# Kernel tuning notes

Hardware: AMD Instinct MI355X
Metric: run time of the kernel (lower is better)

The kernel has to match this reference:

```python
import jax, jax.numpy as jnp
import numpy as np

B, T, C, H = 128, 256, 1024, 64


def setup_inputs() -> dict:
    key = jax.random.key(0)
    k1, k2, k3, k4 = jax.random.split(key, 4)
    # Glorot-ish scale for weights
    s = 1.0 / np.sqrt(C)
    return {
        "x": jax.random.normal(k1, (B, T, C), dtype=jnp.float32),
        "Wk": jax.random.normal(k2, (C, H), dtype=jnp.float32) * s,
        "Wq": jax.random.normal(k3, (C, H), dtype=jnp.float32) * s,
        "Wv": jax.random.normal(k4, (C, H), dtype=jnp.float32) * s,
    }


def reference(x, Wk, Wq, Wv):
    # Projections (no bias, matching use_bias=False)
    k = jnp.einsum("btc,ch->bth", x, Wk)  # [B,T,H]
    q = jnp.einsum("btc,ch->bth", x, Wq)
    v = jnp.einsum("btc,ch->bth", x, Wv)
    scale = k.shape[-1] ** -0.5
    wei = jnp.einsum("bth,bsh->bts", q, k) * scale  # [B,T,T]
    t = x.shape[1]
    causal = jnp.tril(jnp.ones((t, t), dtype=bool))
    wei = jnp.where(causal, wei, -jnp.inf)
    wei = jax.nn.softmax(wei, axis=-1)
    # dropout is identity at inference
    out = jnp.einsum("bts,bsh->bth", wei, v)  # [B,T,H]
    return out
```

## Files before the change

### kernel.cpp

```cpp
#include <hip/hip_runtime.h>
#include <hip/hip_bf16.h>

typedef __bf16 v8bf __attribute__((ext_vector_type(8)));
typedef float f32x16 __attribute__((ext_vector_type(16)));
typedef unsigned int uint;
typedef unsigned short ushort;

#define GLOAD16(gsrc, ldst)                                                       \
  __builtin_amdgcn_global_load_lds(                                               \
      (const __attribute__((address_space(1))) unsigned int*)(gsrc),              \
      (__attribute__((address_space(3))) unsigned int*)(ldst), 16, 0, 0)

__device__ inline f32x16 zero16() {
  f32x16 z;
#pragma unroll
  for (int i = 0; i < 16; i++) z[i] = 0.f;
  return z;
}

__device__ inline uint pack_bf16(float a, float b) {
  union { __bf16 h[2]; uint u; } c;
  c.h[0] = (__bf16)a;
  c.h[1] = (__bf16)b;
  return c.u;
}

__global__ void prep_wt(const float* __restrict__ Wq, const float* __restrict__ Wk,
                        const float* __restrict__ Wv, char* __restrict__ Wt_s) {
  __shared__ __bf16 tile[64][74];
  const int mat = blockIdx.x >> 4;
  const int c0 = (blockIdx.x & 15) * 64;
  const float* src = (mat == 0) ? Wq : (mat == 1) ? Wk : Wv;
  const int t = threadIdx.x;
  {
    const int r = t >> 2;
    const int ch = (t & 3) * 16;
    const float4* s4 = (const float4*)(src + (size_t)(c0 + r) * 64 + ch);
#pragma unroll
    for (int j = 0; j < 4; j++) {
      float4 f = s4[j];
      tile[r][ch + 4 * j + 0] = (__bf16)f.x;
      tile[r][ch + 4 * j + 1] = (__bf16)f.y;
      tile[r][ch + 4 * j + 2] = (__bf16)f.z;
      tile[r][ch + 4 * j + 3] = (__bf16)f.w;
    }
  }
  __syncthreads();
  const int h = t >> 2;
  const int cc = (t & 3) * 16;
  union { __bf16 o[16]; uint4 u[2]; } pk;
#pragma unroll
  for (int j = 0; j < 16; j++) pk.o[j] = tile[cc + j][h];
  const int n = mat * 64 + h;
  char* base = Wt_s + (size_t)n * 2048 + (c0 >> 6) * 128;
  const int bc = cc * 2;
  *(uint4*)(base + ((bc) ^ ((n & 7) << 4))) = pk.u[0];
  *(uint4*)(base + ((bc + 16) ^ ((n & 7) << 4))) = pk.u[1];
}

__launch_bounds__(256, 2)
__global__ void proj_kernel(const float* __restrict__ x, const char* __restrict__ Wt_s,
                            __bf16* __restrict__ KQV) {
  __shared__ char lds[65536];
  char* A0 = lds;
  char* A1 = lds + 8192;
  char* W0 = lds + 16384;
  char* W1 = lds + 40960;

  const int tid = threadIdx.x;
  const int lane = tid & 63;
  const int wave = tid >> 6;
  const int wm = wave >> 1;
  const int wn = wave & 1;
  const int row0 = blockIdx.x * 64;

  const int sr = tid >> 2;
  const int sc = tid & 3;
  const float4* xp = (const float4*)(x + (size_t)(row0 + sr) * 1024 + sc * 16);

  f32x16 acc[3];
#pragma unroll
  for (int i = 0; i < 3; i++) acc[i] = zero16();

  float4 s0[4], s1[4], s2[4], s3[4];

#define SB __builtin_amdgcn_sched_barrier(0)

#define LOADA(rr, t)                                                              \
  {                                                                               \
    _Pragma("unroll") for (int j = 0; j < 4; j++) rr[j] = xp[(t) * 16 + j];       \
  }

#define GW(t, Wbuf)                                                               \
  {                                                                               \
    _Pragma("unroll") for (int j = 0; j < 6; j++) {                               \
      int idx = wave * 64 + j * 256 + lane;                                       \
      GLOAD16(Wt_s + (size_t)(idx >> 3) * 2048 + (t) * 128 + (idx & 7) * 16,      \
              Wbuf + wave * 1024 + j * 4096);                                     \
    }                                                                             \
  }

#define CVTWRITE(rr, Abuf)                                                        \
  {                                                                               \
    union { __bf16 h[16]; uint4 u[2]; } cv;                                       \
    _Pragma("unroll") for (int j = 0; j < 4; j++) {                               \
      cv.h[4 * j + 0] = (__bf16)rr[j].x;                                          \
      cv.h[4 * j + 1] = (__bf16)rr[j].y;                                          \
      cv.h[4 * j + 2] = (__bf16)rr[j].z;                                          \
      cv.h[4 * j + 3] = (__bf16)rr[j].w;                                          \
    }                                                                             \
    *(uint4*)(Abuf + sr * 128 + ((sc * 32) ^ ((sr & 7) << 4))) = cv.u[0];         \
    *(uint4*)(Abuf + sr * 128 + ((sc * 32 + 16) ^ ((sr & 7) << 4))) = cv.u[1];    \
  }

#define MMA(Abuf, Wbuf)                                                           \
  {                                                                               \
    _Pragma("unroll") for (int ks = 0; ks < 4; ks++) {                            \
      int arow = wm * 32 + (lane & 31);                                           \
      int kb = ks * 32 + ((lane >> 5) << 4);                                      \
      v8bf av = *(const v8bf*)(Abuf + arow * 128 + (kb ^ ((arow & 7) << 4)));     \
      _Pragma("unroll") for (int nf = 0; nf < 3; nf++) {                          \
        int brow = wn * 96 + nf * 32 + (lane & 31);                               \
        v8bf bv = *(const v8bf*)(Wbuf + brow * 128 + (kb ^ ((brow & 7) << 4)));   \
        acc[nf] = __builtin_amdgcn_mfma_f32_32x32x16_bf16(av, bv, acc[nf], 0, 0, 0); \
      }                                                                           \
    }                                                                             \
  }

#define BAR4                                                                      \
  do {                                                                            \
    asm volatile("s_waitcnt vmcnt(4) lgkmcnt(0)" ::: "memory");                   \
    __builtin_amdgcn_s_barrier();                                                 \
    SB;                                                                           \
  } while (0)
#define BAR0                                                                      \
  do {                                                                            \
    asm volatile("s_waitcnt vmcnt(0) lgkmcnt(0)" ::: "memory");                   \
    __builtin_amdgcn_s_barrier();                                                 \
    SB;                                                                           \
  } while (0)

#define STEP(T, SI, SC_, ACUR, WCUR, ANXT, WNXT)                                  \
  GW(T + 1, WNXT);                                                                \
  SB;                                                                             \
  LOADA(SI, T + 2);                                                               \
  SB;                                                                             \
  MMA(ACUR, WCUR);                                                                \
  CVTWRITE(SC_, ANXT);                                                            \
  BAR4;

  GW(0, W0);
  SB;
  LOADA(s0, 0);
  LOADA(s1, 1);
  SB;
  CVTWRITE(s0, A0);
  BAR4;

  STEP(0, s2, s1, A0, W0, A1, W1)
  STEP(1, s3, s2, A1, W1, A0, W0)
  STEP(2, s0, s3, A0, W0, A1, W1)
  STEP(3, s1, s0, A1, W1, A0, W0)
  STEP(4, s2, s1, A0, W0, A1, W1)
  STEP(5, s3, s2, A1, W1, A0, W0)
  STEP(6, s0, s3, A0, W0, A1, W1)
  STEP(7, s1, s0, A1, W1, A0, W0)
  STEP(8, s2, s1, A0, W0, A1, W1)
  STEP(9, s3, s2, A1, W1, A0, W0)
  STEP(10, s0, s3, A0, W0, A1, W1)
  STEP(11, s1, s0, A1, W1, A0, W0)
  STEP(12, s2, s1, A0, W0, A1, W1)
  STEP(13, s3, s2, A1, W1, A0, W0)
  GW(15, W1);
  SB;
  MMA(A0, W0);
  CVTWRITE(s3, A1);
  BAR0;
  MMA(A1, W1);

#pragma unroll
  for (int nf = 0; nf < 3; nf++) {
#pragma unroll
    for (int r = 0; r < 16; r++) {
      int row = row0 + wm * 32 + (r & 3) + ((r >> 2) << 3) + ((lane >> 5) << 2);
      int col = wn * 96 + nf * 32 + (lane & 31);
      KQV[(size_t)row * 192 + col] = (__bf16)acc[nf][r];
    }
  }
#undef STEP
#undef BAR4
#undef BAR0
#undef LOADA
#undef GW
#undef CVTWRITE
#undef MMA
#undef SB
}

__launch_bounds__(256, 1)
__global__ void attn_kernel(const __bf16* __restrict__ KQV, float* __restrict__ out) {
  __shared__ uint4 lds4[81920 / 16];
  char* Klds = (char*)lds4;
  char* Vlds = (char*)lds4 + 32768;
  char* Qlds = (char*)lds4 + 65536;

  const int tid = threadIdx.x;
  const int lane = tid & 63;
  const int wave = tid >> 6;
  const int b = blockIdx.x >> 1;
  const int half = blockIdx.x & 1;
  const int bt0 = half * 128;
  const size_t base = (size_t)b * 256 * 192;

  {
    int s = tid;
    const uint4* src = (const uint4*)(KQV + base + (size_t)s * 192 + 64);
#pragma unroll
    for (int i = 0; i < 8; i++) {
      uint4 v = src[i];
      int byte = s * 128 + ((i * 16) ^ ((s & 7) << 4));
      *(uint4*)(Klds + byte) = v;
    }
  }
  {
    int s = tid;
    const uint4* src = (const uint4*)(KQV + base + (size_t)s * 192 + 128);
#pragma unroll
    for (int i = 0; i < 8; i++) {
      uint4 v = src[i];
      const ushort* e = (const ushort*)&v;
#pragma unroll
      for (int j = 0; j < 8; j++) {
        int h = i * 8 + j;
        int byte = h * 512 + ((s * 2) ^ ((h & 7) << 4));
        *(ushort*)(Vlds + byte) = e[j];
      }
    }
  }
#pragma unroll
  for (int i = 0; i < 4; i++) {
    int c = tid + i * 256;
    int r = c >> 3, cc = c & 7;
    uint4 v = *(const uint4*)(KQV + base + (size_t)(bt0 + r) * 192 + cc * 8);
    int byte = r * 128 + ((cc * 16) ^ ((r & 7) << 4));
    *(uint4*)(Qlds + byte) = v;
  }
  __syncthreads();

  const int t0 = bt0 + wave * 32;
  const int tg = t0 + (lane & 31);
  const int nf = (t0 >> 5) + 1;

  f32x16 sacc[8];
#pragma unroll
  for (int sf = 0; sf < 8; sf++) {
    f32x16 sv = zero16();
    if (sf < nf) {
#pragma unroll
      for (int ks = 0; ks < 4; ks++) {
        int kbyte = ks * 32 + ((lane >> 5) << 4);
        int krow = sf * 32 + (lane & 31);
        v8bf a = *(const v8bf*)(Klds + krow * 128 + (kbyte ^ ((krow & 7) << 4)));
        int qrow = wave * 32 + (lane & 31);
        v8bf bq = *(const v8bf*)(Qlds + qrow * 128 + (kbyte ^ ((qrow & 7) << 4)));
        sv = __builtin_amdgcn_mfma_f32_32x32x16_bf16(a, bq, sv, 0, 0, 0);
      }
    }
    sacc[sf] = sv;
  }

  float m = -1e30f;
#pragma unroll
  for (int sf = 0; sf < 8; sf++) {
    if (sf < nf) {
#pragma unroll
      for (int r = 0; r < 16; r++) {
        int sg = sf * 32 + (r & 3) + ((r >> 2) << 3) + ((lane >> 5) << 2);
        float v = sacc[sf][r] * 0.125f;
        v = (sg > tg) ? -1e30f : v;
        sacc[sf][r] = v;
        m = fmaxf(m, v);
      }
    }
  }
  m = fmaxf(m, __shfl_xor(m, 32, 64));
  float l = 0.f;
#pragma unroll
  for (int sf = 0; sf < 8; sf++) {
    if (sf < nf) {
#pragma unroll
      for (int r = 0; r < 16; r++) {
        float p = __expf(sacc[sf][r] - m);
        sacc[sf][r] = p;
        l += p;
      }
    }
  }
  l += __shfl_xor(l, 32, 64);
  float inv = 1.0f / l;

  f32x16 oacc[2];
  oacc[0] = zero16();
  oacc[1] = zero16();
  const bool hiLane = (lane >= 32);
#pragma unroll
  for (int sf = 0; sf < 8; sf++) {
    if (sf < nf) {
      uint w[8], ow[8];
#pragma unroll
      for (int q = 0; q < 4; q++) {
        w[2 * q]     = pack_bf16(sacc[sf][4 * q] * inv,     sacc[sf][4 * q + 1] * inv);
        w[2 * q + 1] = pack_bf16(sacc[sf][4 * q + 2] * inv, sacc[sf][4 * q + 3] * inv);
      }
#pragma unroll
      for (int i = 0; i < 8; i++) ow[i] = (uint)__shfl_xor((int)w[i], 32, 64);
#pragma unroll
      for (int ks = 0; ks < 2; ks++) {
        int bse = 4 * ks;
        union { uint u[4]; v8bf v; } A;
        A.u[0] = hiLane ? ow[bse + 2] : w[bse + 0];
        A.u[1] = hiLane ? ow[bse + 3] : w[bse + 1];
        A.u[2] = hiLane ? w[bse + 2] : ow[bse + 0];
        A.u[3] = hiLane ? w[bse + 3] : ow[bse + 1];
        int sbyte0 = (sf * 32 + ks * 16) * 2 + ((lane >> 5) << 4);
#pragma unroll
        for (int hf = 0; hf < 2; hf++) {
          int vrow = hf * 32 + (lane & 31);
          v8bf bv = *(const v8bf*)(Vlds + vrow * 512 + (sbyte0 ^ ((vrow & 7) << 4)));
          oacc[hf] = __builtin_amdgcn_mfma_f32_32x32x16_bf16(A.v, bv, oacc[hf], 0, 0, 0);
        }
      }
    }
  }

#pragma unroll
  for (int hf = 0; hf < 2; hf++) {
#pragma unroll
    for (int r = 0; r < 16; r++) {
      int t = t0 + (r & 3) + ((r >> 2) << 3) + ((lane >> 5) << 2);
      int h = hf * 32 + (lane & 31);
      out[((size_t)b * 256 + t) * 64 + h] = oacc[hf][r];
    }
  }
}

extern "C" void kernel_launch(void* const* d_in, const int* in_sizes, int n_in,
                              void* d_out, int out_size, void* d_ws, size_t ws_size,
                              hipStream_t stream) {
  const float* x  = (const float*)d_in[0];
  const float* Wk = (const float*)d_in[1];
  const float* Wq = (const float*)d_in[2];
  const float* Wv = (const float*)d_in[3];
  float* out = (float*)d_out;

  __bf16* KQV = (__bf16*)d_ws;
  char* Wt_s  = (char*)d_ws + (size_t)32768 * 192 * 2;

  prep_wt<<<48, 256, 0, stream>>>(Wq, Wk, Wv, Wt_s);
  proj_kernel<<<512, 256, 0, stream>>>(x, Wt_s, KQV);
  attn_kernel<<<256, 256, 0, stream>>>(KQV, out);
}
```

Measured before the change: 45.67 us.

## Split projection output into separate Q, pre-swizzled K, and V buffers

The projection kernel now writes Q, K and V to separate arrays, with K stored in the LDS-swizzled layout the attention kernel expects. The attention kernel then copies K into LDS with direct global-to-LDS loads, holds Q fragments in registers instead of staging them in LDS, and shrinks LDS to 64KB with no fixed occupancy bound. The goal is less LDS traffic and staging work in attention and possibly two blocks per CU. In exchange the projection epilogue does scattered 2-byte swizzled stores and has more branching.

Result: slower. 47.75 us (+4.6%).

```diff
diff --git a/kernel.cpp b/kernel.cpp
--- a/kernel.cpp
+++ b/kernel.cpp
@@ -60,7 +60,8 @@
 
 __launch_bounds__(256, 2)
 __global__ void proj_kernel(const float* __restrict__ x, const char* __restrict__ Wt_s,
-                            __bf16* __restrict__ KQV) {
+                            __bf16* __restrict__ Qa, char* __restrict__ Ka,
+                            __bf16* __restrict__ Va) {
   __shared__ char lds[65536];
   char* A0 = lds;
   char* A1 = lds + 8192;
@@ -180,11 +181,21 @@
 
 #pragma unroll
   for (int nf = 0; nf < 3; nf++) {
+    const int colb = wn * 96 + nf * 32;
 #pragma unroll
     for (int r = 0; r < 16; r++) {
-      int row = row0 + wm * 32 + (r & 3) + ((r >> 2) << 3) + ((lane >> 5) << 2);
-      int col = wn * 96 + nf * 32 + (lane & 31);
-      KQV[(size_t)row * 192 + col] = (__bf16)acc[nf][r];
+      int g = row0 + wm * 32 + (r & 3) + ((r >> 2) << 3) + ((lane >> 5) << 2);
+      __bf16 val = (__bf16)acc[nf][r];
+      if (colb < 64) {
+        Qa[(size_t)g * 64 + colb + (lane & 31)] = val;
+      } else if (colb < 128) {
+        int h = colb - 64 + (lane & 31);
+        int s = g & 255, bb = g >> 8;
+        int byte = s * 128 + ((h * 2) ^ ((s & 7) << 4));
+        *(__bf16*)(Ka + (size_t)bb * 32768 + byte) = val;
+      } else {
+        Va[(size_t)g * 64 + colb - 128 + (lane & 31)] = val;
+      }
     }
   }
 #undef STEP
@@ -197,12 +208,12 @@
 #undef SB
 }
 
-__launch_bounds__(256, 1)
-__global__ void attn_kernel(const __bf16* __restrict__ KQV, float* __restrict__ out) {
-  __shared__ uint4 lds4[81920 / 16];
-  char* Klds = (char*)lds4;
-  char* Vlds = (char*)lds4 + 32768;
-  char* Qlds = (char*)lds4 + 65536;
+__launch_bounds__(256)
+__global__ void attn_kernel(const __bf16* __restrict__ Qa, const char* __restrict__ Ka,
+                            const __bf16* __restrict__ Va, float* __restrict__ out) {
+  __shared__ char lds[65536];
+  char* Klds = lds;
+  char* Vlds = lds + 32768;
 
   const int tid = threadIdx.x;
   const int lane = tid & 63;
@@ -210,21 +221,24 @@
   const int b = blockIdx.x >> 1;
   const int half = blockIdx.x & 1;
   const int bt0 = half * 128;
-  const size_t base = (size_t)b * 256 * 192;
-
+
+  v8bf bq[4];
+  {
+    const __bf16* qsrc = Qa + (size_t)(b * 256 + bt0 + wave * 32 + (lane & 31)) * 64 +
+                         ((lane >> 5) << 3);
+#pragma unroll
+    for (int ks = 0; ks < 4; ks++) bq[ks] = *(const v8bf*)(qsrc + ks * 16);
+  }
+
+  {
+    const char* ksrc = Ka + (size_t)b * 32768 + wave * 1024 + lane * 16;
+#pragma unroll
+    for (int i = 0; i < 8; i++)
+      GLOAD16(ksrc + i * 4096, Klds + wave * 1024 + i * 4096);
+  }
   {
     int s = tid;
-    const uint4* src = (const uint4*)(KQV + base + (size_t)s * 192 + 64);
-#pragma unroll
-    for (int i = 0; i < 8; i++) {
-      uint4 v = src[i];
-      int byte = s * 128 + ((i * 16) ^ ((s & 7) << 4));
-      *(uint4*)(Klds + byte) = v;
-    }
-  }
-  {
-    int s = tid;
-    const uint4* src = (const uint4*)(KQV + base + (size_t)s * 192 + 128);
+    const uint4* src = (const uint4*)(Va + (size_t)(b * 256 + s) * 64);
 #pragma unroll
     for (int i = 0; i < 8; i++) {
       uint4 v = src[i];
@@ -237,14 +251,6 @@
       }
     }
   }
-#pragma unroll
-  for (int i = 0; i < 4; i++) {
-    int c = tid + i * 256;
-    int r = c >> 3, cc = c & 7;
-    uint4 v = *(const uint4*)(KQV + base + (size_t)(bt0 + r) * 192 + cc * 8);
-    int byte = r * 128 + ((cc * 16) ^ ((r & 7) << 4));
-    *(uint4*)(Qlds + byte) = v;
-  }
   __syncthreads();
 
   const int t0 = bt0 + wave * 32;
@@ -261,9 +267,7 @@
         int kbyte = ks * 32 + ((lane >> 5) << 4);
         int krow = sf * 32 + (lane & 31);
         v8bf a = *(const v8bf*)(Klds + krow * 128 + (kbyte ^ ((krow & 7) << 4)));
-        int qrow = wave * 32 + (lane & 31);
-        v8bf bq = *(const v8bf*)(Qlds + qrow * 128 + (kbyte ^ ((qrow & 7) << 4)));
-        sv = __builtin_amdgcn_mfma_f32_32x32x16_bf16(a, bq, sv, 0, 0, 0);
+        sv = __builtin_amdgcn_mfma_f32_32x32x16_bf16(a, bq[ks], sv, 0, 0, 0);
       }
     }
     sacc[sf] = sv;
@@ -353,10 +357,12 @@
   const float* Wv = (const float*)d_in[3];
   float* out = (float*)d_out;
 
-  __bf16* KQV = (__bf16*)d_ws;
-  char* Wt_s  = (char*)d_ws + (size_t)32768 * 192 * 2;
+  __bf16* Qa = (__bf16*)d_ws;
+  char* Ka   = (char*)d_ws + 4194304;
+  __bf16* Va = (__bf16*)((char*)d_ws + 8388608);
+  char* Wt_s = (char*)d_ws + 12582912;
 
   prep_wt<<<48, 256, 0, stream>>>(Wq, Wk, Wv, Wt_s);
-  proj_kernel<<<512, 256, 0, stream>>>(x, Wt_s, KQV);
-  attn_kernel<<<256, 256, 0, stream>>>(KQV, out);
-}
+  proj_kernel<<<512, 256, 0, stream>>>(x, Wt_s, Qa, Ka, Va);
+  attn_kernel<<<256, 256, 0, stream>>>(Qa, Ka, Va, out);
+}
```
